# Performance work log

Hardware: AMD Instinct MI355X
Metric: run time of the kernel (lower is better)

Reference implementation:

```python
import jax, jax.numpy as jnp
import numpy as np

B, L, C = 16, 4096, 9          # batch, max chars, max candidate spans per char (2+3+4)
DI, DO, V = 512, 128, 96       # char hidden, attention/pos-embed dim, pos-BEM vocab


def setup_inputs() -> dict:
    key = jax.random.key(0)
    k0, k1, k2, k3, k4, k5 = jax.random.split(key, 6)
    input_context = jax.random.normal(k0, (B, L, DI), jnp.float32)
    W = jax.random.normal(k1, (DO, DI), jnp.float32) / np.sqrt(DI).astype(np.float32)
    pos_embed = jax.random.normal(k2, (V, DO), jnp.float32)
    cand_idx = jax.random.randint(k3, (B, L, C), 0, V, dtype=jnp.int32)
    cand_mask = jax.random.randint(k4, (B, L, C), 0, 2, dtype=jnp.int32).astype(bool)
    word_seq_len = jax.random.randint(k5, (B,), L // 2, L + 1, dtype=jnp.int32)
    return {
        'input_context': input_context,
        'W': W,
        'pos_embed': pos_embed,
        'cand_idx': cand_idx,
        'cand_mask': cand_mask,
        'word_seq_len': word_seq_len,
    }


def reference(input_context, W, pos_embed, cand_idx, cand_mask, word_seq_len):
    # 'general' attention: score_c = cand_c . (W x_char)
    q = jnp.einsum('bld,od->blo', input_context, W)          # [B, L, DO]
    cand = pos_embed[cand_idx]                               # [B, L, C, DO] gather
    scores = jnp.einsum('blco,blo->blc', cand, q)            # [B, L, C]
    neg = jnp.finfo(scores.dtype).min
    attn = jax.nn.softmax(jnp.where(cand_mask, scores, neg), axis=-1)
    ctx = jnp.einsum('blc,blco->blo', attn, cand)            # [B, L, DO]
    # chars with no matched candidate -> zeros(output_size); pad beyond seq_len -> zeros
    has_cand = cand_mask.any(axis=-1, keepdims=True)         # [B, L, 1]
    in_len = jnp.arange(L, dtype=word_seq_len.dtype)[None, :, None] < word_seq_len[:, None, None]
    return jnp.where(has_cand & in_len, ctx, jnp.zeros((), ctx.dtype))
```

## Files before the change

kernel.cpp:

```cpp
#include <hip/hip_runtime.h>
#include <hip/hip_bf16.h>
#include <hip/hip_fp16.h>
#include <cfloat>

#define BB   16
#define LL   4096
#define CC   9
#define DIN  512
#define DOUT 128
#define VV   96

#define PWLD 520
#define PELD 136

typedef _Float16 h2 __attribute__((ext_vector_type(2)));

#if defined(__has_builtin)
#if __has_builtin(__builtin_amdgcn_fdot2)
#define FDOT2(a, b, c) __builtin_amdgcn_fdot2((a), (b), (c), false)
#endif
#endif
#ifndef FDOT2
__device__ __forceinline__ float FDOT2(h2 a, h2 b, float c) {
    return c + (float)a[0] * (float)b[0] + (float)a[1] * (float)b[1];
}
#endif

__device__ __forceinline__ h2 pack_h2(float lo, float hi) {
    return __builtin_bit_cast(h2, __builtin_amdgcn_cvt_pkrtz(lo, hi));
}

__global__ __launch_bounds__(128)
void pw_kernel(const float* __restrict__ W,
               const float* __restrict__ PE,
               __half*      __restrict__ PW,
               __half*      __restrict__ PEh)
{
    const int v = blockIdx.x;
    const int k = blockIdx.y * 128 + threadIdx.x;
    const float* per = PE + v * DOUT;
    float a = 0.f;
    #pragma unroll 8
    for (int o = 0; o < DOUT; ++o)
        a = fmaf(per[o], W[(size_t)o * DIN + k], a);
    PW[(size_t)v * DIN + k] = __float2half_rn(a);
    if (blockIdx.y == 0)
        PEh[(size_t)v * DOUT + threadIdx.x] = __float2half_rn(per[threadIdx.x]);
}

__global__ __launch_bounds__(1024, 4)
void attn_kernel(const float*  __restrict__ X,
                 const __half* __restrict__ PW,
                 const __half* __restrict__ PEh,
                 const int*    __restrict__ CIDX,
                 const int*    __restrict__ CMASK,
                 const int*    __restrict__ SLEN,
                 float*        __restrict__ OUT)
{
    __shared__ __half lds_pw[VV * PWLD];
    __shared__ __half lds_pe[VV * PELD];

    const int t = threadIdx.x;

    #pragma unroll
    for (int it = 0; it < 6; ++it) {
        int chunk = t + it * 1024;
        int v = chunk >> 6, kq = chunk & 63;
        uint4 d = *(const uint4*)(PW + (size_t)v * DIN + kq * 8);
        *(uint4*)&lds_pw[v * PWLD + kq * 8] = d;
    }
    {
        if (t < 1536) {
            int v = t >> 4, kq = t & 15;
            *(uint4*)&lds_pe[v * PELD + kq * 8] =
                *(const uint4*)(PEh + (size_t)v * DOUT + kq * 8);
        }
        int c2 = t + 1024;
        if (c2 < 1536) {
            int v2 = c2 >> 4, k2 = c2 & 15;
            *(uint4*)&lds_pe[v2 * PELD + k2 * 8] =
                *(const uint4*)(PEh + (size_t)v2 * DOUT + k2 * 8);
        }
    }
    __syncthreads();

    const int lane = t & 63;
    const int il   = lane & 15;
    const int slot = t >> 4;
    const int rowbase = blockIdx.x * 256;

    int    ci[2][CC];
    int    vmw[2][CC];
    float4 xf[2][8];

    {
        const int row = rowbase + slot;
        #pragma unroll
        for (int c = 0; c < CC; ++c) ci[0][c]  = CIDX[(size_t)row * CC + c];
        #pragma unroll
        for (int c = 0; c < CC; ++c) vmw[0][c] = CMASK[(size_t)row * CC + c];
        const float* xr = X + (size_t)row * DIN;
        #pragma unroll
        for (int j = 0; j < 4; ++j) {
            xf[0][j * 2 + 0] = *(const float4*)(xr + il * 8 + 128 * j);
            xf[0][j * 2 + 1] = *(const float4*)(xr + il * 8 + 128 * j + 4);
        }
    }

    #pragma unroll
    for (int i = 0; i < 4; ++i) {
        const int cur = i & 1;
        const int nxt = cur ^ 1;

        if (i < 3) {
            const int rown = rowbase + (i + 1) * 64 + slot;
            #pragma unroll
            for (int c = 0; c < CC; ++c) ci[nxt][c]  = CIDX[(size_t)rown * CC + c];
            #pragma unroll
            for (int c = 0; c < CC; ++c) vmw[nxt][c] = CMASK[(size_t)rown * CC + c];
            const float* xrn = X + (size_t)rown * DIN;
            #pragma unroll
            for (int j = 0; j < 4; ++j) {
                xf[nxt][j * 2 + 0] = *(const float4*)(xrn + il * 8 + 128 * j);
                xf[nxt][j * 2 + 1] = *(const float4*)(xrn + il * 8 + 128 * j + 4);
            }
        }

        const int row = rowbase + i * 64 + slot;
        const int  b     = row >> 12;
        const int  l     = row & (LL - 1);
        const bool inlen = l < SLEN[b];

        h2 xh[16];
        #pragma unroll
        for (int q = 0; q < 8; ++q) {
            xh[q * 2 + 0] = pack_h2(xf[cur][q].x, xf[cur][q].y);
            xh[q * 2 + 1] = pack_h2(xf[cur][q].z, xf[cur][q].w);
        }

        float sc[CC];
        #pragma unroll
        for (int c = 0; c < CC; ++c) sc[c] = 0.f;
        #pragma unroll
        for (int j = 0; j < 4; ++j) {
            #pragma unroll
            for (int c = 0; c < CC; ++c) {
                uint4 pwb = *(const uint4*)&lds_pw[ci[cur][c] * PWLD + j * 128 + il * 8];
                h2 p0 = __builtin_bit_cast(h2, pwb.x);
                h2 p1 = __builtin_bit_cast(h2, pwb.y);
                h2 p2 = __builtin_bit_cast(h2, pwb.z);
                h2 p3 = __builtin_bit_cast(h2, pwb.w);
                float s = sc[c];
                s = FDOT2(xh[j * 4 + 0], p0, s);
                s = FDOT2(xh[j * 4 + 1], p1, s);
                s = FDOT2(xh[j * 4 + 2], p2, s);
                s = FDOT2(xh[j * 4 + 3], p3, s);
                sc[c] = s;
            }
        }
        #pragma unroll
        for (int c = 0; c < CC; ++c) {
            float s = sc[c];
            s += __shfl_xor(s, 1);
            s += __shfl_xor(s, 2);
            s += __shfl_xor(s, 4);
            s += __shfl_xor(s, 8);
            sc[c] = s;
        }

        bool any = false;
        float mx = -FLT_MAX;
        #pragma unroll
        for (int c = 0; c < CC; ++c)
            if (vmw[cur][c]) { mx = fmaxf(mx, sc[c]); any = true; }
        float e[CC];
        float den = 0.f;
        #pragma unroll
        for (int c = 0; c < CC; ++c) {
            e[c] = vmw[cur][c] ? __expf(sc[c] - mx) : 0.f;
            den += e[c];
        }
        const float scale = (any && inlen) ? (1.f / den) : 0.f;

        float o[8];
        #pragma unroll
        for (int j = 0; j < 8; ++j) o[j] = 0.f;
        #pragma unroll
        for (int c = 0; c < CC; ++c) {
            const float w = e[c];
            uint4 peb = *(const uint4*)&lds_pe[ci[cur][c] * PELD + il * 8];
            h2 q0 = __builtin_bit_cast(h2, peb.x);
            h2 q1 = __builtin_bit_cast(h2, peb.y);
            h2 q2 = __builtin_bit_cast(h2, peb.z);
            h2 q3 = __builtin_bit_cast(h2, peb.w);
            o[0] = fmaf(w, (float)q0[0], o[0]); o[1] = fmaf(w, (float)q0[1], o[1]);
            o[2] = fmaf(w, (float)q1[0], o[2]); o[3] = fmaf(w, (float)q1[1], o[3]);
            o[4] = fmaf(w, (float)q2[0], o[4]); o[5] = fmaf(w, (float)q2[1], o[5]);
            o[6] = fmaf(w, (float)q3[0], o[6]); o[7] = fmaf(w, (float)q3[1], o[7]);
        }

        float* op = OUT + (size_t)row * DOUT + il * 8;
        *(float4*)op       = make_float4(o[0] * scale, o[1] * scale, o[2] * scale, o[3] * scale);
        *(float4*)(op + 4) = make_float4(o[4] * scale, o[5] * scale, o[6] * scale, o[7] * scale);
    }
}

extern "C" void kernel_launch(void* const* d_in, const int* in_sizes, int n_in,
                              void* d_out, int out_size, void* d_ws, size_t ws_size,
                              hipStream_t stream) {
    const float* X  = (const float*)d_in[0];
    const float* W  = (const float*)d_in[1];
    const float* PE = (const float*)d_in[2];
    const int*   CI = (const int*)d_in[3];
    const int*   CM = (const int*)d_in[4];
    const int*   SL = (const int*)d_in[5];
    float* OUT = (float*)d_out;
    __half* PW  = (__half*)d_ws;
    __half* PEh = (__half*)d_ws + (size_t)VV * DIN;

    hipLaunchKernelGGL(pw_kernel, dim3(VV, 4), dim3(128), 0, stream, W, PE, PW, PEh);

    const int rows = BB * LL;
    hipLaunchKernelGGL(attn_kernel, dim3(rows / 256), dim3(1024), 0, stream,
                       X, PW, PEh, CI, CM, SL, OUT);
}
```

Baseline: 45.81 us.

## Skip X loads for dead rows and prefetch X before LDS table fill

Loads candidate indices, masks and sequence length for all four rows up front and computes a per-row alive flag. X rows are only fetched for rows that have a candidate and lie within the sequence length, and dead rows write zeros directly. The first X load is issued before the LDS table fill so it overlaps it, and scheduling barriers enforce a two-buffer prefetch order. The launch-bounds occupancy hint is removed, and holding all indices and masks in registers raises register pressure.

```diff
diff --git a/kernel.cpp b/kernel.cpp
--- a/kernel.cpp
+++ b/kernel.cpp
@@ -48,7 +48,7 @@
         PEh[(size_t)v * DOUT + threadIdx.x] = __float2half_rn(per[threadIdx.x]);
 }
 
-__global__ __launch_bounds__(1024, 4)
+__global__ __launch_bounds__(1024)
 void attn_kernel(const float*  __restrict__ X,
                  const __half* __restrict__ PW,
                  const __half* __restrict__ PEh,
@@ -60,7 +60,41 @@
     __shared__ __half lds_pw[VV * PWLD];
     __shared__ __half lds_pe[VV * PELD];
 
-    const int t = threadIdx.x;
+    const int t    = threadIdx.x;
+    const int il   = t & 15;
+    const int slot = t >> 4;
+    const int rowbase = blockIdx.x * 256;
+
+    int  ci[4][CC];
+    int  vm[4][CC];
+    bool alive[4];
+    #pragma unroll
+    for (int I = 0; I < 4; ++I) {
+        const int r = rowbase + I * 64 + slot;
+        #pragma unroll
+        for (int c = 0; c < CC; ++c) ci[I][c] = CIDX[(size_t)r * CC + c];
+        #pragma unroll
+        for (int c = 0; c < CC; ++c) vm[I][c] = CMASK[(size_t)r * CC + c];
+        int any = 0;
+        #pragma unroll
+        for (int c = 0; c < CC; ++c) any |= vm[I][c];
+        const int b = r >> 12, l = r & (LL - 1);
+        alive[I] = (any != 0) && (l < SLEN[b]);
+    }
+
+    float4 XA[8], XB[8];
+
+#define XISSUE(BUF, I)                                                        \
+    if (alive[I]) {                                                           \
+        const float* _xr = X + (size_t)(rowbase + (I) * 64 + slot) * DIN + il * 8; \
+        _Pragma("unroll")                                                     \
+        for (int j = 0; j < 4; ++j) {                                         \
+            BUF[2 * j]     = *(const float4*)(_xr + 128 * j);                 \
+            BUF[2 * j + 1] = *(const float4*)(_xr + 128 * j + 4);             \
+        }                                                                     \
+    }
+
+    XISSUE(XA, 0)
 
     #pragma unroll
     for (int it = 0; it < 6; ++it) {
@@ -69,140 +103,106 @@
         uint4 d = *(const uint4*)(PW + (size_t)v * DIN + kq * 8);
         *(uint4*)&lds_pw[v * PWLD + kq * 8] = d;
     }
-    {
-        if (t < 1536) {
-            int v = t >> 4, kq = t & 15;
-            *(uint4*)&lds_pe[v * PELD + kq * 8] =
-                *(const uint4*)(PEh + (size_t)v * DOUT + kq * 8);
-        }
+    if (t < 1536) {
+        int v = t >> 4, kq = t & 15;
+        *(uint4*)&lds_pe[v * PELD + kq * 8] =
+            *(const uint4*)(PEh + (size_t)v * DOUT + kq * 8);
+    }
+    if (t < 512) {
         int c2 = t + 1024;
-        if (c2 < 1536) {
-            int v2 = c2 >> 4, k2 = c2 & 15;
-            *(uint4*)&lds_pe[v2 * PELD + k2 * 8] =
-                *(const uint4*)(PEh + (size_t)v2 * DOUT + k2 * 8);
-        }
+        int v2 = c2 >> 4, k2 = c2 & 15;
+        *(uint4*)&lds_pe[v2 * PELD + k2 * 8] =
+            *(const uint4*)(PEh + (size_t)v2 * DOUT + k2 * 8);
     }
     __syncthreads();
 
-    const int lane = t & 63;
-    const int il   = lane & 15;
-    const int slot = t >> 4;
-    const int rowbase = blockIdx.x * 256;
-
-    int    ci[2][CC];
-    int    vmw[2][CC];
-    float4 xf[2][8];
-
-    {
-        const int row = rowbase + slot;
-        #pragma unroll
-        for (int c = 0; c < CC; ++c) ci[0][c]  = CIDX[(size_t)row * CC + c];
-        #pragma unroll
-        for (int c = 0; c < CC; ++c) vmw[0][c] = CMASK[(size_t)row * CC + c];
-        const float* xr = X + (size_t)row * DIN;
-        #pragma unroll
-        for (int j = 0; j < 4; ++j) {
-            xf[0][j * 2 + 0] = *(const float4*)(xr + il * 8 + 128 * j);
-            xf[0][j * 2 + 1] = *(const float4*)(xr + il * 8 + 128 * j + 4);
-        }
-    }
-
-    #pragma unroll
-    for (int i = 0; i < 4; ++i) {
-        const int cur = i & 1;
-        const int nxt = cur ^ 1;
-
-        if (i < 3) {
-            const int rown = rowbase + (i + 1) * 64 + slot;
-            #pragma unroll
-            for (int c = 0; c < CC; ++c) ci[nxt][c]  = CIDX[(size_t)rown * CC + c];
-            #pragma unroll
-            for (int c = 0; c < CC; ++c) vmw[nxt][c] = CMASK[(size_t)rown * CC + c];
-            const float* xrn = X + (size_t)rown * DIN;
-            #pragma unroll
-            for (int j = 0; j < 4; ++j) {
-                xf[nxt][j * 2 + 0] = *(const float4*)(xrn + il * 8 + 128 * j);
-                xf[nxt][j * 2 + 1] = *(const float4*)(xrn + il * 8 + 128 * j + 4);
-            }
-        }
-
-        const int row = rowbase + i * 64 + slot;
-        const int  b     = row >> 12;
-        const int  l     = row & (LL - 1);
-        const bool inlen = l < SLEN[b];
-
-        h2 xh[16];
-        #pragma unroll
-        for (int q = 0; q < 8; ++q) {
-            xh[q * 2 + 0] = pack_h2(xf[cur][q].x, xf[cur][q].y);
-            xh[q * 2 + 1] = pack_h2(xf[cur][q].z, xf[cur][q].w);
-        }
-
-        float sc[CC];
-        #pragma unroll
-        for (int c = 0; c < CC; ++c) sc[c] = 0.f;
-        #pragma unroll
-        for (int j = 0; j < 4; ++j) {
-            #pragma unroll
-            for (int c = 0; c < CC; ++c) {
-                uint4 pwb = *(const uint4*)&lds_pw[ci[cur][c] * PWLD + j * 128 + il * 8];
-                h2 p0 = __builtin_bit_cast(h2, pwb.x);
-                h2 p1 = __builtin_bit_cast(h2, pwb.y);
-                h2 p2 = __builtin_bit_cast(h2, pwb.z);
-                h2 p3 = __builtin_bit_cast(h2, pwb.w);
-                float s = sc[c];
-                s = FDOT2(xh[j * 4 + 0], p0, s);
-                s = FDOT2(xh[j * 4 + 1], p1, s);
-                s = FDOT2(xh[j * 4 + 2], p2, s);
-                s = FDOT2(xh[j * 4 + 3], p3, s);
-                sc[c] = s;
-            }
-        }
-        #pragma unroll
-        for (int c = 0; c < CC; ++c) {
-            float s = sc[c];
-            s += __shfl_xor(s, 1);
-            s += __shfl_xor(s, 2);
-            s += __shfl_xor(s, 4);
-            s += __shfl_xor(s, 8);
-            sc[c] = s;
-        }
-
-        bool any = false;
-        float mx = -FLT_MAX;
-        #pragma unroll
-        for (int c = 0; c < CC; ++c)
-            if (vmw[cur][c]) { mx = fmaxf(mx, sc[c]); any = true; }
-        float e[CC];
-        float den = 0.f;
-        #pragma unroll
-        for (int c = 0; c < CC; ++c) {
-            e[c] = vmw[cur][c] ? __expf(sc[c] - mx) : 0.f;
-            den += e[c];
-        }
-        const float scale = (any && inlen) ? (1.f / den) : 0.f;
-
-        float o[8];
-        #pragma unroll
-        for (int j = 0; j < 8; ++j) o[j] = 0.f;
-        #pragma unroll
-        for (int c = 0; c < CC; ++c) {
-            const float w = e[c];
-            uint4 peb = *(const uint4*)&lds_pe[ci[cur][c] * PELD + il * 8];
-            h2 q0 = __builtin_bit_cast(h2, peb.x);
-            h2 q1 = __builtin_bit_cast(h2, peb.y);
-            h2 q2 = __builtin_bit_cast(h2, peb.z);
-            h2 q3 = __builtin_bit_cast(h2, peb.w);
-            o[0] = fmaf(w, (float)q0[0], o[0]); o[1] = fmaf(w, (float)q0[1], o[1]);
-            o[2] = fmaf(w, (float)q1[0], o[2]); o[3] = fmaf(w, (float)q1[1], o[3]);
-            o[4] = fmaf(w, (float)q2[0], o[4]); o[5] = fmaf(w, (float)q2[1], o[5]);
-            o[6] = fmaf(w, (float)q3[0], o[6]); o[7] = fmaf(w, (float)q3[1], o[7]);
-        }
-
-        float* op = OUT + (size_t)row * DOUT + il * 8;
-        *(float4*)op       = make_float4(o[0] * scale, o[1] * scale, o[2] * scale, o[3] * scale);
-        *(float4*)(op + 4) = make_float4(o[4] * scale, o[5] * scale, o[6] * scale, o[7] * scale);
-    }
+#define COMP(BUF, I) {                                                        \
+    const int row = rowbase + (I) * 64 + slot;                                \
+    float* op = OUT + (size_t)row * DOUT + il * 8;                            \
+    if (!alive[I]) {                                                          \
+        *(float4*)op       = make_float4(0.f, 0.f, 0.f, 0.f);                 \
+        *(float4*)(op + 4) = make_float4(0.f, 0.f, 0.f, 0.f);                 \
+    } else {                                                                  \
+        h2 xh[16];                                                            \
+        _Pragma("unroll")                                                     \
+        for (int q = 0; q < 8; ++q) {                                         \
+            xh[q * 2 + 0] = pack_h2(BUF[q].x, BUF[q].y);                      \
+            xh[q * 2 + 1] = pack_h2(BUF[q].z, BUF[q].w);                      \
+        }                                                                     \
+        float sc[CC];                                                         \
+        _Pragma("unroll")                                                     \
+        for (int c = 0; c < CC; ++c) sc[c] = 0.f;                             \
+        _Pragma("unroll")                                                     \
+        for (int j = 0; j < 4; ++j) {                                         \
+            _Pragma("unroll")                                                 \
+            for (int c = 0; c < CC; ++c) {                                    \
+                uint4 pwb = *(const uint4*)&lds_pw[ci[I][c] * PWLD + j * 128 + il * 8]; \
+                h2 p0 = __builtin_bit_cast(h2, pwb.x);                        \
+                h2 p1 = __builtin_bit_cast(h2, pwb.y);                        \
+                h2 p2 = __builtin_bit_cast(h2, pwb.z);                        \
+                h2 p3 = __builtin_bit_cast(h2, pwb.w);                        \
+                float s = sc[c];                                              \
+                s = FDOT2(xh[j * 4 + 0], p0, s);                              \
+                s = FDOT2(xh[j * 4 + 1], p1, s);                              \
+                s = FDOT2(xh[j * 4 + 2], p2, s);                              \
+                s = FDOT2(xh[j * 4 + 3], p3, s);                              \
+                sc[c] = s;                                                    \
+            }                                                                 \
+        }                                                                     \
+        _Pragma("unroll")                                                     \
+        for (int c = 0; c < CC; ++c) {                                        \
+            float s = sc[c];                                                  \
+            s += __shfl_xor(s, 1);                                            \
+            s += __shfl_xor(s, 2);                                            \
+            s += __shfl_xor(s, 4);                                            \
+            s += __shfl_xor(s, 8);                                            \
+            sc[c] = s;                                                        \
+        }                                                                     \
+        float mx = -FLT_MAX;                                                  \
+        _Pragma("unroll")                                                     \
+        for (int c = 0; c < CC; ++c)                                          \
+            if (vm[I][c]) mx = fmaxf(mx, sc[c]);                              \
+        float e[CC], den = 0.f;                                               \
+        _Pragma("unroll")                                                     \
+        for (int c = 0; c < CC; ++c) {                                        \
+            e[c] = vm[I][c] ? __expf(sc[c] - mx) : 0.f;                       \
+            den += e[c];                                                      \
+        }                                                                     \
+        const float scale = 1.f / den;                                        \
+        float o[8];                                                           \
+        _Pragma("unroll")                                                     \
+        for (int j = 0; j < 8; ++j) o[j] = 0.f;                               \
+        _Pragma("unroll")                                                     \
+        for (int c = 0; c < CC; ++c) {                                        \
+            const float w = e[c];                                             \
+            uint4 peb = *(const uint4*)&lds_pe[ci[I][c] * PELD + il * 8];     \
+            h2 q0 = __builtin_bit_cast(h2, peb.x);                            \
+            h2 q1 = __builtin_bit_cast(h2, peb.y);                            \
+            h2 q2 = __builtin_bit_cast(h2, peb.z);                            \
+            h2 q3 = __builtin_bit_cast(h2, peb.w);                            \
+            o[0] = fmaf(w, (float)q0[0], o[0]); o[1] = fmaf(w, (float)q0[1], o[1]); \
+            o[2] = fmaf(w, (float)q1[0], o[2]); o[3] = fmaf(w, (float)q1[1], o[3]); \
+            o[4] = fmaf(w, (float)q2[0], o[4]); o[5] = fmaf(w, (float)q2[1], o[5]); \
+            o[6] = fmaf(w, (float)q3[0], o[6]); o[7] = fmaf(w, (float)q3[1], o[7]); \
+        }                                                                     \
+        *(float4*)op       = make_float4(o[0] * scale, o[1] * scale, o[2] * scale, o[3] * scale); \
+        *(float4*)(op + 4) = make_float4(o[4] * scale, o[5] * scale, o[6] * scale, o[7] * scale); \
+    }                                                                         \
+}
+
+    XISSUE(XB, 1)
+    __builtin_amdgcn_sched_barrier(0);
+    COMP(XA, 0)
+    XISSUE(XA, 2)
+    __builtin_amdgcn_sched_barrier(0);
+    COMP(XB, 1)
+    XISSUE(XB, 3)
+    __builtin_amdgcn_sched_barrier(0);
+    COMP(XA, 2)
+    COMP(XB, 3)
+
+#undef XISSUE
+#undef COMP
 }
 
 extern "C" void kernel_launch(void* const* d_in, const int* in_sizes, int n_in,
```

After: 75.86 us. 1.66x slower.
